# Performance work log

Measured on AMD Instinct MI355X. Metric: run time of the kernel, lower is better.

Reference implementation:

```python
import jax, jax.numpy as jnp
import numpy as np

NUM_NODES = 4096
EMBED_DIM = 64
IN_DIM = 256
OUT_DIM = 256
BATCH = 32


def setup_inputs() -> dict:
    key = jax.random.key(0)
    k1, k2, k3 = jax.random.split(key, 3)
    x = jax.random.normal(k1, (BATCH, NUM_NODES, IN_DIM), dtype=jnp.float32)
    node_ids = jnp.arange(NUM_NODES, dtype=jnp.int64)
    emb_table = jax.random.normal(k2, (NUM_NODES, EMBED_DIM), dtype=jnp.float32) * 0.1
    W = jax.random.normal(k3, (IN_DIM, OUT_DIM), dtype=jnp.float32) * (1.0 / np.sqrt(IN_DIM))
    b = jnp.zeros((OUT_DIM,), dtype=jnp.float32)
    return {"x": x, "node_ids": node_ids, "emb_table": emb_table, "W": W, "b": b}


def reference(x, node_ids, emb_table, W, b):
    # Embedding lookup for node ids -> [N, E]
    E = emb_table[node_ids]
    # Adaptive adjacency from embeddings: softmax(relu(E E^T)) over neighbors
    logits = jax.nn.relu(jnp.einsum("ne,me->nm", E, E))  # [N, N]
    adj = jax.nn.softmax(logits, axis=-1)
    # Graph convolution: aggregate neighbor features, then linear + relu
    h = jnp.einsum("nm,bmd->bnd", adj, x)          # [B, N, in_dim]
    out = jax.nn.relu(jnp.einsum("bnd,do->bno", h, W) + b)  # [B, N, out_dim]
    return out
```

## Files before the change

### kernel.cpp

```cpp
#include <hip/hip_runtime.h>

#define NN   4096
#define ED   64
#define DIN  256
#define DOUT 256
#define NB   32

typedef __attribute__((ext_vector_type(8))) short bf16x8;
typedef __attribute__((ext_vector_type(4))) float f32x4;

__device__ __forceinline__ unsigned short f2bf(float f) {
    union { float f; unsigned u; } v; v.f = f;
    unsigned r = v.u + 0x7FFF + ((v.u >> 16) & 1);
    return (unsigned short)(r >> 16);
}
__device__ __forceinline__ float bf2f(unsigned short s) {
    union { unsigned u; float f; } v; v.u = ((unsigned)s) << 16;
    return v.f;
}

#define GLDS16(g, l) __builtin_amdgcn_global_load_lds( \
    (const __attribute__((address_space(1))) void*)(g), \
    (__attribute__((address_space(3))) void*)(l), 16, 0, 0)

__device__ __forceinline__ void fma4(float4& d, float s, const float4& v) {
    d.x = fmaf(s, v.x, d.x);
    d.y = fmaf(s, v.y, d.y);
    d.z = fmaf(s, v.z, d.z);
    d.w = fmaf(s, v.w, d.w);
}

__global__ void k_gather(const float* __restrict__ emb, const int* __restrict__ ids,
                         unsigned short* __restrict__ Ebf, float* __restrict__ Z) {
    int n = blockIdx.x;
    int e = threadIdx.x;
    int id = ids[n];
    id = id < 0 ? 0 : (id >= NN ? NN - 1 : id);
    Ebf[(size_t)n * ED + e] = f2bf(emb[(size_t)id * ED + e]);
    if (e == 0) Z[n] = 0.0f;
}

__global__ __launch_bounds__(256) void k_logits(const unsigned short* __restrict__ Ebf,
                                                unsigned short* __restrict__ P,
                                                float* __restrict__ Z) {
    __shared__ __align__(16) float Ea[ED][64 + 4];
    __shared__ __align__(16) float Eb[ED][64 + 4];
    const int tid = threadIdx.x;
    const int ty = tid >> 4, tx = tid & 15;
    const int rb = blockIdx.x, cb = blockIdx.y;

    #pragma unroll
    for (int k = 0; k < 4; ++k) {
        int l = tid + k * 256;
        int row = l >> 4;
        int kq = (l & 15) * 4;
        ushort4 va = *(const ushort4*)&Ebf[(size_t)(rb * 64 + row) * ED + kq];
        Ea[kq + 0][row] = bf2f(va.x); Ea[kq + 1][row] = bf2f(va.y);
        Ea[kq + 2][row] = bf2f(va.z); Ea[kq + 3][row] = bf2f(va.w);
        ushort4 vb = *(const ushort4*)&Ebf[(size_t)(cb * 64 + row) * ED + kq];
        Eb[kq + 0][row] = bf2f(vb.x); Eb[kq + 1][row] = bf2f(vb.y);
        Eb[kq + 2][row] = bf2f(vb.z); Eb[kq + 3][row] = bf2f(vb.w);
    }
    __syncthreads();

    float4 acc[4] = {};
    #pragma unroll
    for (int k = 0; k < ED; ++k) {
        float4 ar = *(const float4*)&Ea[k][ty * 4];
        float4 br = *(const float4*)&Eb[k][tx * 4];
        fma4(acc[0], ar.x, br);
        fma4(acc[1], ar.y, br);
        fma4(acc[2], ar.z, br);
        fma4(acc[3], ar.w, br);
    }

    float rsum[4];
    #pragma unroll
    for (int i = 0; i < 4; ++i) {
        float4 v = acc[i];
        v.x = __expf(fmaxf(v.x, 0.f)); v.y = __expf(fmaxf(v.y, 0.f));
        v.z = __expf(fmaxf(v.z, 0.f)); v.w = __expf(fmaxf(v.w, 0.f));
        rsum[i] = v.x + v.y + v.z + v.w;
        ushort4 s;
        s.x = f2bf(v.x); s.y = f2bf(v.y); s.z = f2bf(v.z); s.w = f2bf(v.w);
        size_t n = (size_t)(rb * 64 + ty * 4 + i);
        *(ushort4*)&P[n * NN + cb * 64 + tx * 4] = s;
    }
    #pragma unroll
    for (int i = 0; i < 4; ++i) {
        #pragma unroll
        for (int off = 1; off < 16; off <<= 1)
            rsum[i] += __shfl_xor(rsum[i], off);
        if (tx == 0) atomicAdd(&Z[rb * 64 + ty * 4 + i], rsum[i]);
    }
}

__global__ void k_wt(const float* __restrict__ W, unsigned short* __restrict__ WT) {
    int m = blockIdx.x;
    int k = threadIdx.x;
    WT[(size_t)m * DIN + k] = f2bf(W[(size_t)k * DOUT + m]);
}

__global__ __launch_bounds__(256) void k_y(const unsigned short* __restrict__ WT,
                                           const float* __restrict__ x,
                                           unsigned short* __restrict__ yT) {
    __shared__ __align__(16) short As[128 * 32];
    __shared__ __align__(16) short Bs[128 * 32];
    const int tid = threadIdx.x;
    const int lane = tid & 63, w = tid >> 6;
    const int wr = (w >> 1) * 64, wc = (w & 1) * 64;
    const int fr = lane & 15, fq = lane >> 4;
    const int m0 = blockIdx.x * 128;
    const int n0 = blockIdx.y * 128;
    const int b  = blockIdx.z;
    const float* xb = x + (size_t)b * NN * DIN;
    const int brow = tid >> 1, bh = (tid & 1) * 16;

    f32x4 acc[4][4];
    #pragma unroll
    for (int i = 0; i < 4; ++i)
        #pragma unroll
        for (int j = 0; j < 4; ++j) acc[i][j] = (f32x4){0.f, 0.f, 0.f, 0.f};

    for (int k0 = 0; k0 < DIN; k0 += 32) {
        __syncthreads();
        #pragma unroll
        for (int i = 0; i < 2; ++i) {
            int idx = (w * 2 + i) * 512 + lane * 8;
            int row = idx >> 5, kk = idx & 31;
            GLDS16(WT + (size_t)(m0 + row) * DIN + k0 + kk, &As[(w * 2 + i) * 512]);
        }
        float fv[16];
        *(float4*)&fv[0]  = *(const float4*)&xb[(size_t)(n0 + brow) * DIN + k0 + bh + 0];
        *(float4*)&fv[4]  = *(const float4*)&xb[(size_t)(n0 + brow) * DIN + k0 + bh + 4];
        *(float4*)&fv[8]  = *(const float4*)&xb[(size_t)(n0 + brow) * DIN + k0 + bh + 8];
        *(float4*)&fv[12] = *(const float4*)&xb[(size_t)(n0 + brow) * DIN + k0 + bh + 12];
        unsigned u[8];
        #pragma unroll
        for (int j = 0; j < 8; ++j)
            u[j] = (unsigned)f2bf(fv[2 * j]) | ((unsigned)f2bf(fv[2 * j + 1]) << 16);
        *(uint4*)&Bs[brow * 32 + bh]     = make_uint4(u[0], u[1], u[2], u[3]);
        *(uint4*)&Bs[brow * 32 + bh + 8] = make_uint4(u[4], u[5], u[6], u[7]);
        __syncthreads();

        bf16x8 a[4], bb[4];
        #pragma unroll
        for (int mi = 0; mi < 4; ++mi)
            a[mi] = *(const bf16x8*)&As[(wr + mi * 16 + fr) * 32 + fq * 8];
        #pragma unroll
        for (int ni = 0; ni < 4; ++ni)
            bb[ni] = *(const bf16x8*)&Bs[(wc + ni * 16 + fr) * 32 + fq * 8];
        #pragma unroll
        for (int mi = 0; mi < 4; ++mi)
            #pragma unroll
            for (int ni = 0; ni < 4; ++ni)
                acc[mi][ni] = __builtin_amdgcn_mfma_f32_16x16x32_bf16(
                    a[mi], bb[ni], acc[mi][ni], 0, 0, 0);
    }

    unsigned short* yb = yT + (size_t)b * DOUT * NN;
    #pragma unroll
    for (int mi = 0; mi < 4; ++mi)
        #pragma unroll
        for (int ni = 0; ni < 4; ++ni)
            #pragma unroll
            for (int r = 0; r < 4; ++r) {
                int row = m0 + wr + mi * 16 + fq * 4 + r;
                int col = n0 + wc + ni * 16 + fr;
                yb[(size_t)row * NN + col] = f2bf(acc[mi][ni][r]);
            }
}

__global__ __launch_bounds__(512, 2) void k_gcn(const unsigned short* __restrict__ adj,
                                                const unsigned short* __restrict__ yT,
                                                const float* __restrict__ bias,
                                                const float* __restrict__ Z,
                                                float* __restrict__ out) {
    __shared__ __align__(16) char smem[131072];

    const int tid  = threadIdx.x;
    const int lane = tid & 63, wid = tid >> 6;
    const int fr = lane & 15, fq = lane >> 4;
    const int wr = wid >> 2, wc = wid & 3;
    const int m0 = blockIdx.x * 256;
    const int by = blockIdx.y;

    const char* Apanel = (const char*)(adj + (size_t)m0 * NN);
    const char* Bpanel = (const char*)(yT + (size_t)by * DOUT * NN);

    #define STAGE_HALF(gpan, ktb, KS, ldsb)                                      \
        { _Pragma("unroll")                                                      \
          for (int h = 0; h < 2; ++h) {                                          \
              int r = h * 128 + wid * 16 + (lane >> 2);                          \
              int gcol = (((lane & 3) ^ ((r >> 1) & 3)) << 4);                   \
              GLDS16((gpan) + (size_t)r * 8192 + (ktb) + (KS) * 64 + gcol,       \
                     (ldsb) + (KS) * 16384 + h * 8192 + wid * 1024);             \
          } }

    STAGE_HALF(Apanel, 0,   0, smem);
    STAGE_HALF(Bpanel, 0,   0, smem + 32768);
    STAGE_HALF(Apanel, 0,   1, smem);
    STAGE_HALF(Bpanel, 0,   1, smem + 32768);
    STAGE_HALF(Apanel, 128, 0, smem + 65536);
    STAGE_HALF(Bpanel, 128, 0, smem + 65536 + 32768);

    f32x4 acc[8][4];
    #pragma unroll
    for (int i = 0; i < 8; ++i)
        #pragma unroll
        for (int j = 0; j < 4; ++j) acc[i][j] = (f32x4){0.f, 0.f, 0.f, 0.f};

    const int chunksw = ((fq ^ ((fr >> 1) & 3)) << 4);
    const int arow = (wr * 128 + fr) * 64 + chunksw;
    const int brow = (wc * 64  + fr) * 64 + chunksw;

    #define READ_A(dst, RB0, KS)                                                 \
        _Pragma("unroll")                                                        \
        for (int mi = 0; mi < 4; ++mi)                                           \
            dst[mi] = *(const bf16x8*)(bufA + (KS) * 16384 + arow + ((RB0) + mi) * 1024);
    #define READ_B(dst, KS)                                                      \
        _Pragma("unroll")                                                        \
        for (int ni = 0; ni < 4; ++ni)                                           \
            dst[ni] = *(const bf16x8*)(bufB + (KS) * 16384 + brow + ni * 1024);
    #define MFMA16(AOFF, Aset, Bset)                                             \
        __builtin_amdgcn_s_setprio(1);                                           \
        _Pragma("unroll")                                                        \
        for (int mi = 0; mi < 4; ++mi)                                           \
            _Pragma("unroll")                                                    \
            for (int ni = 0; ni < 4; ++ni)                                       \
                acc[(AOFF) + mi][ni] = __builtin_amdgcn_mfma_f32_16x16x32_bf16(  \
                    Aset[mi], Bset[ni], acc[(AOFF) + mi][ni], 0, 0, 0);          \
        __builtin_amdgcn_s_setprio(0);

    asm volatile("s_waitcnt vmcnt(8)" ::: "memory");
    asm volatile("s_barrier" ::: "memory");

    for (int t = 0; t < 64; ++t) {
        char* bufA  = smem + (t & 1) * 65536;
        char* bufB  = bufA + 32768;
        char* nbufA = smem + ((t + 1) & 1) * 65536;
        char* nbufB = nbufA + 32768;
        bf16x8 Af[4], Bf[4];

        READ_B(Bf, 0);
        READ_A(Af, 0, 0);
        if (t + 1 < 64) STAGE_HALF(Apanel, (t + 1) * 128, 1, nbufA);
        asm volatile("s_barrier" ::: "memory");
        asm volatile("s_waitcnt lgkmcnt(0)" ::: "memory");
        __builtin_amdgcn_sched_barrier(0);
        MFMA16(0, Af, Bf);
        asm volatile("s_barrier" ::: "memory");

        READ_A(Af, 4, 0);
        if (t + 1 < 64) STAGE_HALF(Bpanel, (t + 1) * 128, 1, nbufB);
        asm volatile("s_barrier" ::: "memory");
        asm volatile("s_waitcnt lgkmcnt(0)" ::: "memory");
        __builtin_amdgcn_sched_barrier(0);
        MFMA16(4, Af, Bf);
        if (t < 63) { asm volatile("s_waitcnt vmcnt(8)" ::: "memory"); }
        else        { asm volatile("s_waitcnt vmcnt(0)" ::: "memory"); }
        asm volatile("s_barrier" ::: "memory");

        READ_B(Bf, 1);
        READ_A(Af, 0, 1);
        if (t + 2 < 64) STAGE_HALF(Apanel, (t + 2) * 128, 0, bufA);
        asm volatile("s_barrier" ::: "memory");
        asm volatile("s_waitcnt lgkmcnt(0)" ::: "memory");
        __builtin_amdgcn_sched_barrier(0);
        MFMA16(0, Af, Bf);
        asm volatile("s_barrier" ::: "memory");

        READ_A(Af, 4, 1);
        if (t + 2 < 64) STAGE_HALF(Bpanel, (t + 2) * 128, 0, bufB);
        asm volatile("s_barrier" ::: "memory");
        asm volatile("s_waitcnt lgkmcnt(0)" ::: "memory");
        __builtin_amdgcn_sched_barrier(0);
        MFMA16(4, Af, Bf);
        if (t < 62)       { asm volatile("s_waitcnt vmcnt(8)" ::: "memory"); }
        else if (t == 62) { asm volatile("s_waitcnt vmcnt(4)" ::: "memory"); }
        asm volatile("s_barrier" ::: "memory");
    }

    float bv[4];
    #pragma unroll
    for (int ni = 0; ni < 4; ++ni) bv[ni] = bias[wc * 64 + ni * 16 + fr];

    #pragma unroll
    for (int am = 0; am < 8; ++am) {
        const int node = m0 + wr * 128 + am * 16 + fq * 4;
        float4 zq = *(const float4*)&Z[node];
        float iz[4] = {1.0f / zq.x, 1.0f / zq.y, 1.0f / zq.z, 1.0f / zq.w};
        #pragma unroll
        for (int ni = 0; ni < 4; ++ni) {
            const int dcol = wc * 64 + ni * 16 + fr;
            #pragma unroll
            for (int rr = 0; rr < 4; ++rr) {
                float vv = acc[am][ni][rr] * iz[rr] + bv[ni];
                out[((size_t)by * NN + node + rr) * DOUT + dcol] = fmaxf(vv, 0.f);
            }
        }
    }
    #undef STAGE_HALF
    #undef READ_A
    #undef READ_B
    #undef MFMA16
}

extern "C" void kernel_launch(void* const* d_in, const int* in_sizes, int n_in,
                              void* d_out, int out_size, void* d_ws, size_t ws_size,
                              hipStream_t stream) {
    const float* x    = (const float*)d_in[0];
    const int*   ids  = (const int*)d_in[1];
    const float* emb  = (const float*)d_in[2];
    const float* W    = (const float*)d_in[3];
    const float* bias = (const float*)d_in[4];
    float* out = (float*)d_out;

    char* ws = (char*)d_ws;
    unsigned short* Pbf = (unsigned short*)ws;
    unsigned short* Ebf = (unsigned short*)(ws + 33554432);
    float*          Z   = (float*)(ws + 33554432 + 524288);
    unsigned short* WT  = (unsigned short*)(ws + 33554432 + 1048576);
    unsigned short* yT  = (unsigned short*)(ws + 33554432 + 1048576 + 131072);

    k_gather <<<NN, ED, 0, stream>>>(emb, ids, Ebf, Z);
    k_logits <<<dim3(NN / 64, NN / 64), 256, 0, stream>>>(Ebf, Pbf, Z);
    k_wt     <<<DOUT, DIN, 0, stream>>>(W, WT);
    k_y      <<<dim3(DOUT / 128, NN / 128, NB), 256, 0, stream>>>(WT, x, yT);
    k_gcn    <<<dim3(16, 32), 512, 0, stream>>>(Pbf, yT, bias, Z, out);
}
```

Baseline: 321.5 us.

## Use MFMA for logits kernel and 32x32 MFMA with fragment-native LDS layout in GCN

```diff
diff --git a/kernel.cpp b/kernel.cpp
--- a/kernel.cpp
+++ b/kernel.cpp
@@ -6,8 +6,9 @@
 #define DOUT 256
 #define NB   32
 
-typedef __attribute__((ext_vector_type(8))) short bf16x8;
-typedef __attribute__((ext_vector_type(4))) float f32x4;
+typedef __attribute__((ext_vector_type(8)))  short bf16x8;
+typedef __attribute__((ext_vector_type(4)))  float f32x4;
+typedef __attribute__((ext_vector_type(16))) float f32x16;
 
 __device__ __forceinline__ unsigned short f2bf(float f) {
     union { float f; unsigned u; } v; v.f = f;
@@ -22,13 +23,6 @@
 #define GLDS16(g, l) __builtin_amdgcn_global_load_lds( \
     (const __attribute__((address_space(1))) void*)(g), \
     (__attribute__((address_space(3))) void*)(l), 16, 0, 0)
-
-__device__ __forceinline__ void fma4(float4& d, float s, const float4& v) {
-    d.x = fmaf(s, v.x, d.x);
-    d.y = fmaf(s, v.y, d.y);
-    d.z = fmaf(s, v.z, d.z);
-    d.w = fmaf(s, v.w, d.w);
-}
 
 __global__ void k_gather(const float* __restrict__ emb, const int* __restrict__ ids,
                          unsigned short* __restrict__ Ebf, float* __restrict__ Z) {
@@ -43,56 +37,80 @@
 __global__ __launch_bounds__(256) void k_logits(const unsigned short* __restrict__ Ebf,
                                                 unsigned short* __restrict__ P,
                                                 float* __restrict__ Z) {
-    __shared__ __align__(16) float Ea[ED][64 + 4];
-    __shared__ __align__(16) float Eb[ED][64 + 4];
+    __shared__ __align__(16) char sm[32768];
     const int tid = threadIdx.x;
-    const int ty = tid >> 4, tx = tid & 15;
+    const int lane = tid & 63, wid = tid >> 6;
+    const int fr = lane & 15, fq = lane >> 4;
+    const int wr = wid >> 1, wc = wid & 1;
     const int rb = blockIdx.x, cb = blockIdx.y;
-
-    #pragma unroll
-    for (int k = 0; k < 4; ++k) {
-        int l = tid + k * 256;
-        int row = l >> 4;
-        int kq = (l & 15) * 4;
-        ushort4 va = *(const ushort4*)&Ebf[(size_t)(rb * 64 + row) * ED + kq];
-        Ea[kq + 0][row] = bf2f(va.x); Ea[kq + 1][row] = bf2f(va.y);
-        Ea[kq + 2][row] = bf2f(va.z); Ea[kq + 3][row] = bf2f(va.w);
-        ushort4 vb = *(const ushort4*)&Ebf[(size_t)(cb * 64 + row) * ED + kq];
-        Eb[kq + 0][row] = bf2f(vb.x); Eb[kq + 1][row] = bf2f(vb.y);
-        Eb[kq + 2][row] = bf2f(vb.z); Eb[kq + 3][row] = bf2f(vb.w);
+    const char* Ep = (const char*)Ebf;
+
+    #pragma unroll
+    for (int i = 0; i < 2; ++i) {
+        int arb = wid * 2 + i;
+        #pragma unroll
+        for (int ks = 0; ks < 2; ++ks) {
+            GLDS16(Ep + (size_t)(rb * 128 + arb * 16 + fr) * 128 + ks * 64 + fq * 16,
+                   sm + arb * 2048 + ks * 1024);
+            GLDS16(Ep + (size_t)(cb * 128 + arb * 16 + fr) * 128 + ks * 64 + fq * 16,
+                   sm + 16384 + arb * 2048 + ks * 1024);
+        }
     }
+    asm volatile("s_waitcnt vmcnt(0)" ::: "memory");
     __syncthreads();
 
-    float4 acc[4] = {};
-    #pragma unroll
-    for (int k = 0; k < ED; ++k) {
-        float4 ar = *(const float4*)&Ea[k][ty * 4];
-        float4 br = *(const float4*)&Eb[k][tx * 4];
-        fma4(acc[0], ar.x, br);
-        fma4(acc[1], ar.y, br);
-        fma4(acc[2], ar.z, br);
-        fma4(acc[3], ar.w, br);
-    }
-
-    float rsum[4];
-    #pragma unroll
-    for (int i = 0; i < 4; ++i) {
-        float4 v = acc[i];
-        v.x = __expf(fmaxf(v.x, 0.f)); v.y = __expf(fmaxf(v.y, 0.f));
-        v.z = __expf(fmaxf(v.z, 0.f)); v.w = __expf(fmaxf(v.w, 0.f));
-        rsum[i] = v.x + v.y + v.z + v.w;
-        ushort4 s;
-        s.x = f2bf(v.x); s.y = f2bf(v.y); s.z = f2bf(v.z); s.w = f2bf(v.w);
-        size_t n = (size_t)(rb * 64 + ty * 4 + i);
-        *(ushort4*)&P[n * NN + cb * 64 + tx * 4] = s;
-    }
-    #pragma unroll
-    for (int i = 0; i < 4; ++i) {
-        #pragma unroll
-        for (int off = 1; off < 16; off <<= 1)
-            rsum[i] += __shfl_xor(rsum[i], off);
-        if (tx == 0) atomicAdd(&Z[rb * 64 + ty * 4 + i], rsum[i]);
-    }
+    bf16x8 Afr[4][2], Bfr[4][2];
+    #pragma unroll
+    for (int mi = 0; mi < 4; ++mi)
+        #pragma unroll
+        for (int ks = 0; ks < 2; ++ks) {
+            Afr[mi][ks] = *(const bf16x8*)(sm + (wr * 4 + mi) * 2048 + ks * 1024 + lane * 16);
+            Bfr[mi][ks] = *(const bf16x8*)(sm + 16384 + (wc * 4 + mi) * 2048 + ks * 1024 + lane * 16);
+        }
+
+    f32x4 acc[4][4];
+    #pragma unroll
+    for (int i = 0; i < 4; ++i)
+        #pragma unroll
+        for (int j = 0; j < 4; ++j) acc[i][j] = (f32x4){0.f, 0.f, 0.f, 0.f};
+    #pragma unroll
+    for (int ks = 0; ks < 2; ++ks)
+        #pragma unroll
+        for (int mi = 0; mi < 4; ++mi)
+            #pragma unroll
+            for (int ni = 0; ni < 4; ++ni)
+                acc[mi][ni] = __builtin_amdgcn_mfma_f32_16x16x32_bf16(
+                    Afr[mi][ks], Bfr[ni][ks], acc[mi][ni], 0, 0, 0);
+
+    float rs[4][4];
+    #pragma unroll
+    for (int mi = 0; mi < 4; ++mi)
+        #pragma unroll
+        for (int r = 0; r < 4; ++r) rs[mi][r] = 0.f;
+
+    #pragma unroll
+    for (int mi = 0; mi < 4; ++mi)
+        #pragma unroll
+        for (int ni = 0; ni < 4; ++ni) {
+            int col = cb * 128 + wc * 64 + ni * 16 + fr;
+            #pragma unroll
+            for (int r = 0; r < 4; ++r) {
+                int row = rb * 128 + wr * 64 + mi * 16 + fq * 4 + r;
+                float v = __expf(fmaxf(acc[mi][ni][r], 0.f));
+                rs[mi][r] += v;
+                P[(size_t)row * NN + col] = f2bf(v);
+            }
+        }
+    #pragma unroll
+    for (int mi = 0; mi < 4; ++mi)
+        #pragma unroll
+        for (int r = 0; r < 4; ++r) {
+            float s = rs[mi][r];
+            #pragma unroll
+            for (int off = 1; off < 16; off <<= 1) s += __shfl_xor(s, off);
+            if (fr == 0)
+                atomicAdd(&Z[rb * 128 + wr * 64 + mi * 16 + fq * 4 + r], s);
+        }
 }
 
 __global__ void k_wt(const float* __restrict__ W, unsigned short* __restrict__ WT) {
@@ -180,7 +198,7 @@
 
     const int tid  = threadIdx.x;
     const int lane = tid & 63, wid = tid >> 6;
-    const int fr = lane & 15, fq = lane >> 4;
+    const int l31 = lane & 31, lhi = lane >> 5;
     const int wr = wid >> 2, wc = wid & 3;
     const int m0 = blockIdx.x * 256;
     const int by = blockIdx.y;
@@ -188,48 +206,60 @@
     const char* Apanel = (const char*)(adj + (size_t)m0 * NN);
     const char* Bpanel = (const char*)(yT + (size_t)by * DOUT * NN);
 
-    #define STAGE_HALF(gpan, ktb, KS, ldsb)                                      \
+    #define STAGE_A_HALF(T, H, buf)                                              \
         { _Pragma("unroll")                                                      \
-          for (int h = 0; h < 2; ++h) {                                          \
-              int r = h * 128 + wid * 16 + (lane >> 2);                          \
-              int gcol = (((lane & 3) ^ ((r >> 1) & 3)) << 4);                   \
-              GLDS16((gpan) + (size_t)r * 8192 + (ktb) + (KS) * 64 + gcol,       \
-                     (ldsb) + (KS) * 16384 + h * 8192 + wid * 1024);             \
+          for (int i = 0; i < 2; ++i) {                                          \
+              int ks = (H) * 2 + i;                                              \
+              GLDS16(Apanel + (size_t)(wid * 32 + l31) * 8192 + (T) * 128        \
+                            + ks * 32 + lhi * 16,                                \
+                     (buf) + ks * 8192 + wid * 1024);                            \
           } }
-
-    STAGE_HALF(Apanel, 0,   0, smem);
-    STAGE_HALF(Bpanel, 0,   0, smem + 32768);
-    STAGE_HALF(Apanel, 0,   1, smem);
-    STAGE_HALF(Bpanel, 0,   1, smem + 32768);
-    STAGE_HALF(Apanel, 128, 0, smem + 65536);
-    STAGE_HALF(Bpanel, 128, 0, smem + 65536 + 32768);
-
-    f32x4 acc[8][4];
-    #pragma unroll
-    for (int i = 0; i < 8; ++i)
-        #pragma unroll
-        for (int j = 0; j < 4; ++j) acc[i][j] = (f32x4){0.f, 0.f, 0.f, 0.f};
-
-    const int chunksw = ((fq ^ ((fr >> 1) & 3)) << 4);
-    const int arow = (wr * 128 + fr) * 64 + chunksw;
-    const int brow = (wc * 64  + fr) * 64 + chunksw;
-
-    #define READ_A(dst, RB0, KS)                                                 \
+    #define STAGE_B_HALF(T, H, buf)                                              \
+        { _Pragma("unroll")                                                      \
+          for (int i = 0; i < 2; ++i) {                                          \
+              int ks = (H) * 2 + i;                                              \
+              GLDS16(Bpanel + (size_t)(wid * 32 + l31) * 8192 + (T) * 128        \
+                            + ks * 32 + lhi * 16,                                \
+                     (buf) + ks * 8192 + wid * 1024);                            \
+          } }
+
+    STAGE_A_HALF(0, 0, smem);
+    STAGE_B_HALF(0, 0, smem + 32768);
+    STAGE_A_HALF(0, 1, smem);
+    STAGE_B_HALF(0, 1, smem + 32768);
+    STAGE_A_HALF(1, 0, smem + 65536);
+    STAGE_B_HALF(1, 0, smem + 65536 + 32768);
+
+    f32x16 acc[4][2];
+    #pragma unroll
+    for (int i = 0; i < 4; ++i)
+        #pragma unroll
+        for (int j = 0; j < 2; ++j)
+            #pragma unroll
+            for (int e = 0; e < 16; ++e) acc[i][j][e] = 0.f;
+
+    #define READ_A(dst, MIB, H)                                                  \
         _Pragma("unroll")                                                        \
-        for (int mi = 0; mi < 4; ++mi)                                           \
-            dst[mi] = *(const bf16x8*)(bufA + (KS) * 16384 + arow + ((RB0) + mi) * 1024);
-    #define READ_B(dst, KS)                                                      \
+        for (int j = 0; j < 4; ++j) {                                            \
+            int mi = (MIB) + (j >> 1), ks = (H) * 2 + (j & 1);                   \
+            dst[j] = *(const bf16x8*)(bufA + ks * 8192 + (wr * 4 + mi) * 1024 + lane * 16); \
+        }
+    #define READ_B(dst, H)                                                       \
         _Pragma("unroll")                                                        \
-        for (int ni = 0; ni < 4; ++ni)                                           \
-            dst[ni] = *(const bf16x8*)(bufB + (KS) * 16384 + brow + ni * 1024);
-    #define MFMA16(AOFF, Aset, Bset)                                             \
+        for (int j = 0; j < 4; ++j) {                                            \
+            int ni = j >> 1, ks = (H) * 2 + (j & 1);                             \
+            dst[j] = *(const bf16x8*)(bufB + ks * 8192 + (wc * 2 + ni) * 1024 + lane * 16); \
+        }
+    #define MFMA8(AOFF, Aset, Bset)                                              \
         __builtin_amdgcn_s_setprio(1);                                           \
         _Pragma("unroll")                                                        \
-        for (int mi = 0; mi < 4; ++mi)                                           \
+        for (int mr = 0; mr < 2; ++mr)                                           \
             _Pragma("unroll")                                                    \
-            for (int ni = 0; ni < 4; ++ni)                                       \
-                acc[(AOFF) + mi][ni] = __builtin_amdgcn_mfma_f32_16x16x32_bf16(  \
-                    Aset[mi], Bset[ni], acc[(AOFF) + mi][ni], 0, 0, 0);          \
+            for (int ni = 0; ni < 2; ++ni)                                       \
+                _Pragma("unroll")                                                \
+                for (int kr = 0; kr < 2; ++kr)                                   \
+                    acc[(AOFF) + mr][ni] = __builtin_amdgcn_mfma_f32_32x32x16_bf16( \
+                        Aset[mr * 2 + kr], Bset[ni * 2 + kr], acc[(AOFF) + mr][ni], 0, 0, 0); \
         __builtin_amdgcn_s_setprio(0);
 
     asm volatile("s_waitcnt vmcnt(8)" ::: "memory");
@@ -244,66 +274,67 @@
 
         READ_B(Bf, 0);
         READ_A(Af, 0, 0);
-        if (t + 1 < 64) STAGE_HALF(Apanel, (t + 1) * 128, 1, nbufA);
+        if (t + 1 < 64) STAGE_A_HALF(t + 1, 1, nbufA);
         asm volatile("s_barrier" ::: "memory");
         asm volatile("s_waitcnt lgkmcnt(0)" ::: "memory");
         __builtin_amdgcn_sched_barrier(0);
-        MFMA16(0, Af, Bf);
-        asm volatile("s_barrier" ::: "memory");
-
-        READ_A(Af, 4, 0);
-        if (t + 1 < 64) STAGE_HALF(Bpanel, (t + 1) * 128, 1, nbufB);
+        MFMA8(0, Af, Bf);
+        asm volatile("s_barrier" ::: "memory");
+
+        READ_A(Af, 2, 0);
+        if (t + 1 < 64) STAGE_B_HALF(t + 1, 1, nbufB);
         asm volatile("s_barrier" ::: "memory");
         asm volatile("s_waitcnt lgkmcnt(0)" ::: "memory");
         __builtin_amdgcn_sched_barrier(0);
-        MFMA16(4, Af, Bf);
+        MFMA8(2, Af, Bf);
         if (t < 63) { asm volatile("s_waitcnt vmcnt(8)" ::: "memory"); }
         else        { asm volatile("s_waitcnt vmcnt(0)" ::: "memory"); }
         asm volatile("s_barrier" ::: "memory");
 
         READ_B(Bf, 1);
         READ_A(Af, 0, 1);
-        if (t + 2 < 64) STAGE_HALF(Apanel, (t + 2) * 128, 0, bufA);
+        if (t + 2 < 64) STAGE_A_HALF(t + 2, 0, bufA);
         asm volatile("s_barrier" ::: "memory");
         asm volatile("s_waitcnt lgkmcnt(0)" ::: "memory");
         __builtin_amdgcn_sched_barrier(0);
-        MFMA16(0, Af, Bf);
-        asm volatile("s_barrier" ::: "memory");
-
-        READ_A(Af, 4, 1);
-        if (t + 2 < 64) STAGE_HALF(Bpanel, (t + 2) * 128, 0, bufB);
+        MFMA8(0, Af, Bf);
+        asm volatile("s_barrier" ::: "memory");
+
+        READ_A(Af, 2, 1);
+        if (t + 2 < 64) STAGE_B_HALF(t + 2, 0, bufB);
         asm volatile("s_barrier" ::: "memory");
         asm volatile("s_waitcnt lgkmcnt(0)" ::: "memory");
         __builtin_amdgcn_sched_barrier(0);
-        MFMA16(4, Af, Bf);
+        MFMA8(2, Af, Bf);
         if (t < 62)       { asm volatile("s_waitcnt vmcnt(8)" ::: "memory"); }
         else if (t == 62) { asm volatile("s_waitcnt vmcnt(4)" ::: "memory"); }
         asm volatile("s_barrier" ::: "memory");
     }
 
-    float bv[4];
-    #pragma unroll
-    for (int ni = 0; ni < 4; ++ni) bv[ni] = bias[wc * 64 + ni * 16 + fr];
-
-    #pragma unroll
-    for (int am = 0; am < 8; ++am) {
-        const int node = m0 + wr * 128 + am * 16 + fq * 4;
-        float4 zq = *(const float4*)&Z[node];
-        float iz[4] = {1.0f / zq.x, 1.0f / zq.y, 1.0f / zq.z, 1.0f / zq.w};
-        #pragma unroll
-        for (int ni = 0; ni < 4; ++ni) {
-            const int dcol = wc * 64 + ni * 16 + fr;
-            #pragma unroll
-            for (int rr = 0; rr < 4; ++rr) {
-                float vv = acc[am][ni][rr] * iz[rr] + bv[ni];
-                out[((size_t)by * NN + node + rr) * DOUT + dcol] = fmaxf(vv, 0.f);
+    #pragma unroll
+    for (int mi = 0; mi < 4; ++mi) {
+        const int mbase = m0 + wr * 128 + mi * 32 + 4 * lhi;
+        #pragma unroll
+        for (int ni = 0; ni < 2; ++ni) {
+            const int dcol = wc * 64 + ni * 32 + l31;
+            const float bv = bias[dcol];
+            #pragma unroll
+            for (int rq = 0; rq < 4; ++rq) {
+                float4 zq = *(const float4*)&Z[mbase + rq * 8];
+                #pragma unroll
+                for (int j = 0; j < 4; ++j) {
+                    int node = mbase + rq * 8 + j;
+                    float vv = acc[mi][ni][rq * 4 + j] * (1.0f / ((float*)&zq)[j]) + bv;
+                    out[((size_t)by * NN + node) * DOUT + dcol] = fmaxf(vv, 0.f);
+                }
             }
         }
     }
-    #undef STAGE_HALF
+    #undef STAGE_A_HALF
+    #undef STAGE_B_HALF
     #undef READ_A
     #undef READ_B
-    #undef MFMA16
+    #undef MFMA8
 }
 
 extern "C" void kernel_launch(void* const* d_in, const int* in_sizes, int n_in,
@@ -324,7 +355,7 @@
     unsigned short* yT  = (unsigned short*)(ws + 33554432 + 1048576 + 131072);
 
     k_gather <<<NN, ED, 0, stream>>>(emb, ids, Ebf, Z);
-    k_logits <<<dim3(NN / 64, NN / 64), 256, 0, stream>>>(Ebf, Pbf, Z);
+    k_logits <<<dim3(NN / 128, NN / 128), 256, 0, stream>>>(Ebf, Pbf, Z);
     k_wt     <<<DOUT, DIN, 0, stream>>>(W, WT);
     k_y      <<<dim3(DOUT / 128, NN / 128, NB), 256, 0, stream>>>(WT, x, yT);
     k_gcn    <<<dim3(16, 32), 512, 0, stream>>>(Pbf, yT, bias, Z, out);
```

New measurement: 369.1 us. 14.8% more time.

## Compute E·Eᵀ logits with bf16 MFMA on 128x128 tiles using direct-to-LDS loads

Applied to the files above, without the earlier changes.

```diff
diff --git a/kernel.cpp b/kernel.cpp
--- a/kernel.cpp
+++ b/kernel.cpp
@@ -6,8 +6,8 @@
 #define DOUT 256
 #define NB   32
 
-typedef __attribute__((ext_vector_type(8))) short bf16x8;
-typedef __attribute__((ext_vector_type(4))) float f32x4;
+typedef __attribute__((ext_vector_type(8)))  short bf16x8;
+typedef __attribute__((ext_vector_type(4)))  float f32x4;
 
 __device__ __forceinline__ unsigned short f2bf(float f) {
     union { float f; unsigned u; } v; v.f = f;
@@ -22,13 +22,6 @@
 #define GLDS16(g, l) __builtin_amdgcn_global_load_lds( \
     (const __attribute__((address_space(1))) void*)(g), \
     (__attribute__((address_space(3))) void*)(l), 16, 0, 0)
-
-__device__ __forceinline__ void fma4(float4& d, float s, const float4& v) {
-    d.x = fmaf(s, v.x, d.x);
-    d.y = fmaf(s, v.y, d.y);
-    d.z = fmaf(s, v.z, d.z);
-    d.w = fmaf(s, v.w, d.w);
-}
 
 __global__ void k_gather(const float* __restrict__ emb, const int* __restrict__ ids,
                          unsigned short* __restrict__ Ebf, float* __restrict__ Z) {
@@ -43,56 +36,80 @@
 __global__ __launch_bounds__(256) void k_logits(const unsigned short* __restrict__ Ebf,
                                                 unsigned short* __restrict__ P,
                                                 float* __restrict__ Z) {
-    __shared__ __align__(16) float Ea[ED][64 + 4];
-    __shared__ __align__(16) float Eb[ED][64 + 4];
+    __shared__ __align__(16) char sm[32768];
     const int tid = threadIdx.x;
-    const int ty = tid >> 4, tx = tid & 15;
+    const int lane = tid & 63, wid = tid >> 6;
+    const int fr = lane & 15, fq = lane >> 4;
+    const int wr = wid >> 1, wc = wid & 1;
     const int rb = blockIdx.x, cb = blockIdx.y;
-
-    #pragma unroll
-    for (int k = 0; k < 4; ++k) {
-        int l = tid + k * 256;
-        int row = l >> 4;
-        int kq = (l & 15) * 4;
-        ushort4 va = *(const ushort4*)&Ebf[(size_t)(rb * 64 + row) * ED + kq];
-        Ea[kq + 0][row] = bf2f(va.x); Ea[kq + 1][row] = bf2f(va.y);
-        Ea[kq + 2][row] = bf2f(va.z); Ea[kq + 3][row] = bf2f(va.w);
-        ushort4 vb = *(const ushort4*)&Ebf[(size_t)(cb * 64 + row) * ED + kq];
-        Eb[kq + 0][row] = bf2f(vb.x); Eb[kq + 1][row] = bf2f(vb.y);
-        Eb[kq + 2][row] = bf2f(vb.z); Eb[kq + 3][row] = bf2f(vb.w);
+    const char* Ep = (const char*)Ebf;
+
+    #pragma unroll
+    for (int i = 0; i < 2; ++i) {
+        int arb = wid * 2 + i;
+        #pragma unroll
+        for (int ks = 0; ks < 2; ++ks) {
+            GLDS16(Ep + (size_t)(rb * 128 + arb * 16 + fr) * 128 + ks * 64 + fq * 16,
+                   sm + arb * 2048 + ks * 1024);
+            GLDS16(Ep + (size_t)(cb * 128 + arb * 16 + fr) * 128 + ks * 64 + fq * 16,
+                   sm + 16384 + arb * 2048 + ks * 1024);
+        }
     }
+    asm volatile("s_waitcnt vmcnt(0)" ::: "memory");
     __syncthreads();
 
-    float4 acc[4] = {};
-    #pragma unroll
-    for (int k = 0; k < ED; ++k) {
-        float4 ar = *(const float4*)&Ea[k][ty * 4];
-        float4 br = *(const float4*)&Eb[k][tx * 4];
-        fma4(acc[0], ar.x, br);
-        fma4(acc[1], ar.y, br);
-        fma4(acc[2], ar.z, br);
-        fma4(acc[3], ar.w, br);
-    }
-
-    float rsum[4];
-    #pragma unroll
-    for (int i = 0; i < 4; ++i) {
-        float4 v = acc[i];
-        v.x = __expf(fmaxf(v.x, 0.f)); v.y = __expf(fmaxf(v.y, 0.f));
-        v.z = __expf(fmaxf(v.z, 0.f)); v.w = __expf(fmaxf(v.w, 0.f));
-        rsum[i] = v.x + v.y + v.z + v.w;
-        ushort4 s;
-        s.x = f2bf(v.x); s.y = f2bf(v.y); s.z = f2bf(v.z); s.w = f2bf(v.w);
-        size_t n = (size_t)(rb * 64 + ty * 4 + i);
-        *(ushort4*)&P[n * NN + cb * 64 + tx * 4] = s;
-    }
-    #pragma unroll
-    for (int i = 0; i < 4; ++i) {
-        #pragma unroll
-        for (int off = 1; off < 16; off <<= 1)
-            rsum[i] += __shfl_xor(rsum[i], off);
-        if (tx == 0) atomicAdd(&Z[rb * 64 + ty * 4 + i], rsum[i]);
-    }
+    bf16x8 Afr[4][2], Bfr[4][2];
+    #pragma unroll
+    for (int mi = 0; mi < 4; ++mi)
+        #pragma unroll
+        for (int ks = 0; ks < 2; ++ks) {
+            Afr[mi][ks] = *(const bf16x8*)(sm + (wr * 4 + mi) * 2048 + ks * 1024 + lane * 16);
+            Bfr[mi][ks] = *(const bf16x8*)(sm + 16384 + (wc * 4 + mi) * 2048 + ks * 1024 + lane * 16);
+        }
+
+    f32x4 acc[4][4];
+    #pragma unroll
+    for (int i = 0; i < 4; ++i)
+        #pragma unroll
+        for (int j = 0; j < 4; ++j) acc[i][j] = (f32x4){0.f, 0.f, 0.f, 0.f};
+    #pragma unroll
+    for (int ks = 0; ks < 2; ++ks)
+        #pragma unroll
+        for (int mi = 0; mi < 4; ++mi)
+            #pragma unroll
+            for (int ni = 0; ni < 4; ++ni)
+                acc[mi][ni] = __builtin_amdgcn_mfma_f32_16x16x32_bf16(
+                    Afr[mi][ks], Bfr[ni][ks], acc[mi][ni], 0, 0, 0);
+
+    float rs[4][4];
+    #pragma unroll
+    for (int mi = 0; mi < 4; ++mi)
+        #pragma unroll
+        for (int r = 0; r < 4; ++r) rs[mi][r] = 0.f;
+
+    #pragma unroll
+    for (int mi = 0; mi < 4; ++mi)
+        #pragma unroll
+        for (int ni = 0; ni < 4; ++ni) {
+            int col = cb * 128 + wc * 64 + ni * 16 + fr;
+            #pragma unroll
+            for (int r = 0; r < 4; ++r) {
+                int row = rb * 128 + wr * 64 + mi * 16 + fq * 4 + r;
+                float v = __expf(fmaxf(acc[mi][ni][r], 0.f));
+                rs[mi][r] += v;
+                P[(size_t)row * NN + col] = f2bf(v);
+            }
+        }
+    #pragma unroll
+    for (int mi = 0; mi < 4; ++mi)
+        #pragma unroll
+        for (int r = 0; r < 4; ++r) {
+            float s = rs[mi][r];
+            #pragma unroll
+            for (int off = 1; off < 16; off <<= 1) s += __shfl_xor(s, off);
+            if (fr == 0)
+                atomicAdd(&Z[rb * 128 + wr * 64 + mi * 16 + fq * 4 + r], s);
+        }
 }
 
 __global__ void k_wt(const float* __restrict__ W, unsigned short* __restrict__ WT) {
@@ -324,7 +341,7 @@
     unsigned short* yT  = (unsigned short*)(ws + 33554432 + 1048576 + 131072);
 
     k_gather <<<NN, ED, 0, stream>>>(emb, ids, Ebf, Z);
-    k_logits <<<dim3(NN / 64, NN / 64), 256, 0, stream>>>(Ebf, Pbf, Z);
+    k_logits <<<dim3(NN / 128, NN / 128), 256, 0, stream>>>(Ebf, Pbf, Z);
     k_wt     <<<DOUT, DIN, 0, stream>>>(W, WT);
     k_y      <<<dim3(DOUT / 128, NN / 128, NB), 256, 0, stream>>>(WT, x, yT);
     k_gcn    <<<dim3(16, 32), 512, 0, stream>>>(Pbf, yT, bias, Z, out);
```

New measurement: 301.8 us. -6.1%, faster.
